# Performance work log

Hardware: AMD Instinct MI355X
Metric: run time of the kernel (lower is better)

## Reference

```python
import jax, jax.numpy as jnp
import numpy as np

B, N, E = 16, 10000, 160000
C_IN, C_SP, C_OUT = 32, 16, 32


def _glorot(key, shape):
    s = float(np.sqrt(6.0 / (shape[0] + shape[1])))
    return jax.random.uniform(key, shape, jnp.float32, -s, s)


def setup_inputs() -> dict:
    key = jax.random.key(0)
    ks = jax.random.split(key, 12)
    X = jax.random.normal(ks[0], (B, N, C_IN), jnp.float32)
    edge_index1 = jax.random.randint(ks[1], (2, E), 0, N)
    edge_weight1 = jax.random.uniform(ks[2], (E,), jnp.float32)
    res_n_id1 = jnp.arange(N)
    edge_index2 = jax.random.randint(ks[3], (2, E), 0, N)
    edge_weight2 = jax.random.uniform(ks[4], (E,), jnp.float32)
    res_n_id2 = jnp.arange(N)
    # conv1 params (in=C_IN, out=C_SP, edge_channels=1, concat=True)
    amp_w1 = _glorot(ks[5], (1, C_IN))            # [edge_ch, in]
    gate_w1 = _glorot(ks[6], (2 * C_IN + 1, 1))   # Linear(2*in+edge_ch, 1)
    gate_b1 = jnp.zeros((1,), jnp.float32)
    w1 = _glorot(ks[7], (2 * C_IN, C_SP))         # concat weight
    b1 = jnp.zeros((C_SP,), jnp.float32)
    # conv2 params (in=C_SP, out=C_OUT)
    amp_w2 = _glorot(ks[8], (1, C_SP))
    gate_w2 = _glorot(ks[9], (2 * C_SP + 1, 1))
    gate_b2 = jnp.zeros((1,), jnp.float32)
    w2 = _glorot(ks[10], (2 * C_SP, C_OUT))
    b2 = jnp.zeros((C_OUT,), jnp.float32)
    return dict(X=X, edge_index1=edge_index1, edge_weight1=edge_weight1, res_n_id1=res_n_id1,
                edge_index2=edge_index2, edge_weight2=edge_weight2, res_n_id2=res_n_id2,
                amp_w1=amp_w1, gate_w1=gate_w1, gate_b1=gate_b1, w1=w1, b1=b1,
                amp_w2=amp_w2, gate_w2=gate_w2, gate_b2=gate_b2, w2=w2, b2=b2)


def _sagela(x_src, x_dst, edge_index, edge_weight, amp_w, gate_w, gate_b, w, b):
    # x_src: [B, N_src, C], x_dst: [B, N_dst, C]
    src, dst = edge_index[0], edge_index[1]
    n_dst = x_dst.shape[1]
    C = x_src.shape[-1]
    x_j = x_src[:, src]                       # [B, E, C] gathered source feats
    x_i = x_dst[:, dst]                       # [B, E, C] gathered target feats
    e = edge_weight[:, None]                  # [E, 1] edge features
    # gate_linear(cat[x_i, x_j, e]) split into three matmuls (same math)
    wg_i, wg_j, wg_e = gate_w[:C], gate_w[C:2 * C], gate_w[2 * C:]
    lamb = jax.nn.sigmoid(x_i @ wg_i + x_j @ wg_j + (e @ wg_e)[None] + gate_b)  # [B, E, 1]
    amp = e @ amp_w                           # [E, C] edge amplification
    msg = amp[None, :, :] * x_j * lamb        # [B, E, C]
    # mean aggregation over incoming edges (scatter-add / count)
    aggr = jnp.zeros((x_src.shape[0], n_dst, C), msg.dtype).at[:, dst].add(msg)
    cnt = jnp.zeros((n_dst,), msg.dtype).at[dst].add(1.0)
    aggr = aggr / jnp.maximum(cnt, 1.0)[None, :, None]
    out = jnp.concatenate([x_dst, aggr], axis=-1) @ w + b  # [B, N_dst, out]
    return out


def reference(X, edge_index1, edge_weight1, res_n_id1, edge_index2, edge_weight2, res_n_id2,
              amp_w1, gate_w1, gate_b1, w1, b1, amp_w2, gate_w2, gate_b2, w2, b2):
    h = _sagela(X, X[:, res_n_id1], edge_index1, edge_weight1, amp_w1, gate_w1, gate_b1, w1, b1)
    h = jax.nn.leaky_relu(h, 0.01)
    out = _sagela(h, h[:, res_n_id2], edge_index2, edge_weight2, amp_w2, gate_w2, gate_b2, w2, b2)
    return out
```

## Files before the change

### kernel.cpp

```cpp
#include <hip/hip_runtime.h>
#include <math.h>

#define B 16
#define N 10000
#define E 160000
#define CAP 96

__device__ __forceinline__ ushort f2bf(float v) {
    uint u = __float_as_uint(v);
    u = (u + 0x7fffu + ((u >> 16) & 1u)) >> 16;
    return (ushort)u;
}
__device__ __forceinline__ float bf2f(ushort u) { return __uint_as_float(((uint)u) << 16); }
__device__ __forceinline__ float bf2f_lo(uint u) { return __uint_as_float(u << 16); }
__device__ __forceinline__ float bf2f_hi(uint u) { return __uint_as_float(u & 0xffff0000u); }
__device__ __forceinline__ float dec_ew(uint u) {
    return ((float)(u >> 14) + 0.5f) * (1.0f / 262144.0f);
}

__global__ __launch_bounds__(256)
void prep_bucket_kernel(const float* __restrict__ X,
                        const float* __restrict__ gate_w1,
                        const int* __restrict__ ei1, const float* __restrict__ ew1,
                        const int* __restrict__ ei2, const float* __restrict__ ew2,
                        const float* __restrict__ w1,
                        const float* __restrict__ w2,
                        ushort* __restrict__ xt,
                        float* __restrict__ gi, float* __restrict__ gj,
                        float* __restrict__ w1T, float* __restrict__ w2T,
                        int* __restrict__ bcount1, uint* __restrict__ bucket1,
                        int* __restrict__ bcount2, uint* __restrict__ bucket2) {
    int gtid = blockIdx.x * 256 + threadIdx.x;
    int gs = gridDim.x * 256;

    for (int t = gtid; t < 2 * E; t += gs) {
        if (t < E) {
            int d = ei1[E + t];
            int pos = atomicAdd(&bcount1[d], 1);
            if (pos < CAP) {
                uint q = (uint)(ew1[t] * 262144.0f);
                if (q > 262143u) q = 262143u;
                bucket1[d * CAP + pos] = (q << 14) | (uint)ei1[t];
            }
        } else {
            int e = t - E;
            int d = ei2[E + e];
            int pos = atomicAdd(&bcount2[d], 1);
            if (pos < CAP) {
                uint q = (uint)(ew2[e] * 262144.0f);
                if (q > 262143u) q = 262143u;
                bucket2[d * CAP + pos] = (q << 14) | (uint)ei2[e];
            }
        }
    }

    for (int tile = blockIdx.x; tile < N / 16; tile += gridDim.x) {
        int n0 = tile * 16;
        int nl = threadIdx.x >> 4, b = threadIdx.x & 15;
        int n = n0 + nl;
        const float4* xr = (const float4*)(X + ((size_t)b * N + n) * 32);
        float pi = 0.f, pj = 0.f;
        union { uint u[16]; uint4 v4[4]; } pk;
        #pragma unroll
        for (int q = 0; q < 8; ++q) {
            float4 v = xr[q];
            pi += v.x * gate_w1[4*q]   + v.y * gate_w1[4*q+1]
                + v.z * gate_w1[4*q+2] + v.w * gate_w1[4*q+3];
            pj += v.x * gate_w1[32+4*q]   + v.y * gate_w1[32+4*q+1]
                + v.z * gate_w1[32+4*q+2] + v.w * gate_w1[32+4*q+3];
            pk.u[2*q]   = (uint)f2bf(v.x) | ((uint)f2bf(v.y) << 16);
            pk.u[2*q+1] = (uint)f2bf(v.z) | ((uint)f2bf(v.w) << 16);
        }
        int r = n0 * 16 + threadIdx.x;
        uint4* dst = (uint4*)(xt + (size_t)r * 32);
        dst[0] = pk.v4[0]; dst[1] = pk.v4[1];
        dst[2] = pk.v4[2]; dst[3] = pk.v4[3];
        gi[r] = pi; gj[r] = pj;
    }

    if (gtid < 1024) {
        w1T[(gtid & 15) * 64 + (gtid >> 4)] = w1[gtid];
        w2T[(gtid & 31) * 32 + (gtid >> 5)] = w2[gtid];
    }
}

__global__ __launch_bounds__(256, 8)
void agg_dense1_kernel(const float* __restrict__ X,
                       const uint4* __restrict__ xt4,
                       const float* __restrict__ gi,
                       const float* __restrict__ gj,
                       const int* __restrict__ bcount,
                       const uint* __restrict__ bucket,
                       const float* __restrict__ gate_w,
                       const float* __restrict__ gate_b,
                       const float* __restrict__ amp_w,
                       const float* __restrict__ w1T,
                       const float* __restrict__ b1,
                       const float* __restrict__ gate_w2,
                       ushort* __restrict__ htb,
                       float* __restrict__ gi2, float* __restrict__ gj2) {
    __shared__ uint  s_eb[CAP];
    __shared__ float s_coef[CAP * 16];
    __shared__ float s_gi[16];
    __shared__ __align__(16) float s_x[16][36];
    __shared__ __align__(16) float s_feat[16][36];
    __shared__ __align__(16) float s_wmT[16 * 68];

    int n = blockIdx.x;
    int tid = threadIdx.x;

    int cnt = bcount[n];
    int deg = cnt < CAP ? cnt : CAP;
    if (tid < CAP / 4)
        ((uint4*)s_eb)[tid] = ((const uint4*)(bucket + (size_t)n * CAP))[tid];
    {
        int o = tid >> 4, k4 = tid & 15;
        *(float4*)&s_wmT[o * 68 + k4 * 4] = ((const float4*)w1T)[o * 16 + k4];
    }
    if (tid < 128) {
        int b = tid >> 3, q = tid & 7;
        *(float4*)&s_x[b][q * 4] = ((const float4*)(X + ((size_t)b * N + n) * 32))[q];
    }
    if (tid < 16) s_gi[tid] = gi[n * 16 + tid] + gate_b[0];
    __syncthreads();

    float wge = gate_w[64];
    for (int p = tid; p < deg * 16; p += 256) {
        int k = p >> 4, b = p & 15;
        uint pr = s_eb[k];
        float w = dec_ew(pr);
        float z = s_gi[b] + gj[(pr & 0x3FFFu) * 16 + b] + w * wge;
        s_coef[p] = w / (1.0f + __expf(-z));
    }
    __syncthreads();

    int wv = tid >> 6, l = tid & 63;
    int c8 = l & 3;
    int b  = 4 * wv + ((l >> 2) & 3);
    int h  = l >> 4;
    uint boff = (uint)b * 4 + c8;
    float a0 = 0.f, a1 = 0.f, a2 = 0.f, a3 = 0.f;
    float a4 = 0.f, a5 = 0.f, a6 = 0.f, a7 = 0.f;
    int k = h;
    for (; k + 4 < deg; k += 16) {
        bool v2 = (k + 8) < deg, v3 = (k + 12) < deg;
        uint i2 = v2 ? (uint)(k + 8) : 0u;
        uint i3 = v3 ? (uint)(k + 12) : 0u;
        uint p0 = s_eb[k], p1 = s_eb[k + 4], p2 = s_eb[i2], p3 = s_eb[i3];
        float c0 = s_coef[(k << 4) | b];
        float c1 = s_coef[((k + 4) << 4) | b];
        float c2 = s_coef[(i2 << 4) | b]; if (!v2) c2 = 0.f;
        float c3 = s_coef[(i3 << 4) | b]; if (!v3) c3 = 0.f;
        uint4 u0 = xt4[(p0 & 0x3FFFu) * 64u + boff];
        uint4 u1 = xt4[(p1 & 0x3FFFu) * 64u + boff];
        uint4 u2 = xt4[(p2 & 0x3FFFu) * 64u + boff];
        uint4 u3 = xt4[(p3 & 0x3FFFu) * 64u + boff];
        a0 += c0 * bf2f_lo(u0.x) + c1 * bf2f_lo(u1.x) + c2 * bf2f_lo(u2.x) + c3 * bf2f_lo(u3.x);
        a1 += c0 * bf2f_hi(u0.x) + c1 * bf2f_hi(u1.x) + c2 * bf2f_hi(u2.x) + c3 * bf2f_hi(u3.x);
        a2 += c0 * bf2f_lo(u0.y) + c1 * bf2f_lo(u1.y) + c2 * bf2f_lo(u2.y) + c3 * bf2f_lo(u3.y);
        a3 += c0 * bf2f_hi(u0.y) + c1 * bf2f_hi(u1.y) + c2 * bf2f_hi(u2.y) + c3 * bf2f_hi(u3.y);
        a4 += c0 * bf2f_lo(u0.z) + c1 * bf2f_lo(u1.z) + c2 * bf2f_lo(u2.z) + c3 * bf2f_lo(u3.z);
        a5 += c0 * bf2f_hi(u0.z) + c1 * bf2f_hi(u1.z) + c2 * bf2f_hi(u2.z) + c3 * bf2f_hi(u3.z);
        a6 += c0 * bf2f_lo(u0.w) + c1 * bf2f_lo(u1.w) + c2 * bf2f_lo(u2.w) + c3 * bf2f_lo(u3.w);
        a7 += c0 * bf2f_hi(u0.w) + c1 * bf2f_hi(u1.w) + c2 * bf2f_hi(u2.w) + c3 * bf2f_hi(u3.w);
    }
    if (k < deg) {
        uint pr = s_eb[k];
        float cc = s_coef[(k << 4) | b];
        uint4 u = xt4[(pr & 0x3FFFu) * 64u + boff];
        a0 += cc * bf2f_lo(u.x); a1 += cc * bf2f_hi(u.x);
        a2 += cc * bf2f_lo(u.y); a3 += cc * bf2f_hi(u.y);
        a4 += cc * bf2f_lo(u.z); a5 += cc * bf2f_hi(u.z);
        a6 += cc * bf2f_lo(u.w); a7 += cc * bf2f_hi(u.w);
    }
    a0 += __shfl_xor(a0, 16, 64); a0 += __shfl_xor(a0, 32, 64);
    a1 += __shfl_xor(a1, 16, 64); a1 += __shfl_xor(a1, 32, 64);
    a2 += __shfl_xor(a2, 16, 64); a2 += __shfl_xor(a2, 32, 64);
    a3 += __shfl_xor(a3, 16, 64); a3 += __shfl_xor(a3, 32, 64);
    a4 += __shfl_xor(a4, 16, 64); a4 += __shfl_xor(a4, 32, 64);
    a5 += __shfl_xor(a5, 16, 64); a5 += __shfl_xor(a5, 32, 64);
    a6 += __shfl_xor(a6, 16, 64); a6 += __shfl_xor(a6, 32, 64);
    a7 += __shfl_xor(a7, 16, 64); a7 += __shfl_xor(a7, 32, 64);
    if (h == 0) {
        float inv = 1.0f / fmaxf((float)cnt, 1.0f);
        int cb = 8 * c8;
        s_feat[b][cb]     = a0 * amp_w[cb]     * inv;
        s_feat[b][cb + 1] = a1 * amp_w[cb + 1] * inv;
        s_feat[b][cb + 2] = a2 * amp_w[cb + 2] * inv;
        s_feat[b][cb + 3] = a3 * amp_w[cb + 3] * inv;
        s_feat[b][cb + 4] = a4 * amp_w[cb + 4] * inv;
        s_feat[b][cb + 5] = a5 * amp_w[cb + 5] * inv;
        s_feat[b][cb + 6] = a6 * amp_w[cb + 6] * inv;
        s_feat[b][cb + 7] = a7 * amp_w[cb + 7] * inv;
    }
    __syncthreads();

    {
        int o = tid & 15, bb = tid >> 4;
        const float4* wr4 = (const float4*)&s_wmT[o * 68];
        const float4* x4  = (const float4*)&s_x[bb][0];
        const float4* f4  = (const float4*)&s_feat[bb][0];
        float d = b1[o];
        #pragma unroll
        for (int q = 0; q < 8; ++q) {
            float4 wvv = wr4[q],    xv = x4[q];
            float4 wf = wr4[8 + q], fv = f4[q];
            d += xv.x * wvv.x + xv.y * wvv.y + xv.z * wvv.z + xv.w * wvv.w;
            d += fv.x * wf.x + fv.y * wf.y + fv.z * wf.z + fv.w * wf.w;
        }
        d = d > 0.0f ? d : 0.01f * d;
        htb[((size_t)n * 16 + bb) * 16 + o] = f2bf(d);
        float pi = d * gate_w2[o];
        float pj = d * gate_w2[16 + o];
        #pragma unroll
        for (int off = 8; off; off >>= 1) {
            pi += __shfl_xor(pi, off, 16);
            pj += __shfl_xor(pj, off, 16);
        }
        if (o == 0) { gi2[n * 16 + bb] = pi; gj2[n * 16 + bb] = pj; }
    }
}

__global__ __launch_bounds__(256, 8)
void agg_dense2_kernel(const uint4* __restrict__ htb4,
                       const float* __restrict__ gi,
                       const float* __restrict__ gj,
                       const int* __restrict__ bcount,
                       const uint* __restrict__ bucket,
                       const float* __restrict__ gate_w,
                       const float* __restrict__ gate_b,
                       const float* __restrict__ amp_w,
                       const float* __restrict__ w2T,
                       const float* __restrict__ b2,
                       float* __restrict__ out) {
    __shared__ uint  s_eb[CAP];
    __shared__ float s_coef[CAP * 16];
    __shared__ float s_gi[16];
    __shared__ __align__(16) float s_x[16][20];
    __shared__ __align__(16) float s_feat[16][20];
    __shared__ __align__(16) float s_wmT[32 * 36];

    int n = blockIdx.x;
    int tid = threadIdx.x;

    int cnt = bcount[n];
    int deg = cnt < CAP ? cnt : CAP;
    if (tid < CAP / 4)
        ((uint4*)s_eb)[tid] = ((const uint4*)(bucket + (size_t)n * CAP))[tid];
    {
        int o = tid >> 3, k4 = tid & 7;
        *(float4*)&s_wmT[o * 36 + k4 * 4] = ((const float4*)w2T)[o * 8 + k4];
    }
    if (tid < 32) {
        uint4 u = htb4[(size_t)n * 32 + tid];
        int b = tid >> 1, cb = (tid & 1) * 8;
        float4 f0, f1;
        f0.x = bf2f_lo(u.x); f0.y = bf2f_hi(u.x);
        f0.z = bf2f_lo(u.y); f0.w = bf2f_hi(u.y);
        f1.x = bf2f_lo(u.z); f1.y = bf2f_hi(u.z);
        f1.z = bf2f_lo(u.w); f1.w = bf2f_hi(u.w);
        *(float4*)&s_x[b][cb]     = f0;
        *(float4*)&s_x[b][cb + 4] = f1;
    }
    if (tid < 16) s_gi[tid] = gi[n * 16 + tid] + gate_b[0];
    __syncthreads();

    float wge = gate_w[32];
    for (int p = tid; p < deg * 16; p += 256) {
        int k = p >> 4, b = p & 15;
        uint pr = s_eb[k];
        float w = dec_ew(pr);
        float z = s_gi[b] + gj[(pr & 0x3FFFu) * 16 + b] + w * wge;
        s_coef[p] = w / (1.0f + __expf(-z));
    }
    __syncthreads();

    int wv = tid >> 6, l = tid & 63;
    int c8 = l & 1;
    int b  = 4 * wv + ((l >> 1) & 3);
    int qd = l >> 3;
    uint boff = (uint)b * 2 + c8;
    float a0 = 0.f, a1 = 0.f, a2 = 0.f, a3 = 0.f;
    float a4 = 0.f, a5 = 0.f, a6 = 0.f, a7 = 0.f;
    int k = qd;
    for (; k + 8 < deg; k += 32) {
        bool v2 = (k + 16) < deg, v3 = (k + 24) < deg;
        uint i2 = v2 ? (uint)(k + 16) : 0u;
        uint i3 = v3 ? (uint)(k + 24) : 0u;
        uint p0 = s_eb[k], p1 = s_eb[k + 8], p2 = s_eb[i2], p3 = s_eb[i3];
        float c0 = s_coef[(k << 4) | b];
        float c1 = s_coef[((k + 8) << 4) | b];
        float c2 = s_coef[(i2 << 4) | b]; if (!v2) c2 = 0.f;
        float c3 = s_coef[(i3 << 4) | b]; if (!v3) c3 = 0.f;
        uint4 u0 = htb4[(p0 & 0x3FFFu) * 32u + boff];
        uint4 u1 = htb4[(p1 & 0x3FFFu) * 32u + boff];
        uint4 u2 = htb4[(p2 & 0x3FFFu) * 32u + boff];
        uint4 u3 = htb4[(p3 & 0x3FFFu) * 32u + boff];
        a0 += c0 * bf2f_lo(u0.x) + c1 * bf2f_lo(u1.x) + c2 * bf2f_lo(u2.x) + c3 * bf2f_lo(u3.x);
        a1 += c0 * bf2f_hi(u0.x) + c1 * bf2f_hi(u1.x) + c2 * bf2f_hi(u2.x) + c3 * bf2f_hi(u3.x);
        a2 += c0 * bf2f_lo(u0.y) + c1 * bf2f_lo(u1.y) + c2 * bf2f_lo(u2.y) + c3 * bf2f_lo(u3.y);
        a3 += c0 * bf2f_hi(u0.y) + c1 * bf2f_hi(u1.y) + c2 * bf2f_hi(u2.y) + c3 * bf2f_hi(u3.y);
        a4 += c0 * bf2f_lo(u0.z) + c1 * bf2f_lo(u1.z) + c2 * bf2f_lo(u2.z) + c3 * bf2f_lo(u3.z);
        a5 += c0 * bf2f_hi(u0.z) + c1 * bf2f_hi(u1.z) + c2 * bf2f_hi(u2.z) + c3 * bf2f_hi(u3.z);
        a6 += c0 * bf2f_lo(u0.w) + c1 * bf2f_lo(u1.w) + c2 * bf2f_lo(u2.w) + c3 * bf2f_lo(u3.w);
        a7 += c0 * bf2f_hi(u0.w) + c1 * bf2f_hi(u1.w) + c2 * bf2f_hi(u2.w) + c3 * bf2f_hi(u3.w);
    }
    if (k < deg) {
        uint pr = s_eb[k];
        float cc = s_coef[(k << 4) | b];
        uint4 u = htb4[(pr & 0x3FFFu) * 32u + boff];
        a0 += cc * bf2f_lo(u.x); a1 += cc * bf2f_hi(u.x);
        a2 += cc * bf2f_lo(u.y); a3 += cc * bf2f_hi(u.y);
        a4 += cc * bf2f_lo(u.z); a5 += cc * bf2f_hi(u.z);
        a6 += cc * bf2f_lo(u.w); a7 += cc * bf2f_hi(u.w);
    }
    a0 += __shfl_xor(a0, 8, 64); a0 += __shfl_xor(a0, 16, 64); a0 += __shfl_xor(a0, 32, 64);
    a1 += __shfl_xor(a1, 8, 64); a1 += __shfl_xor(a1, 16, 64); a1 += __shfl_xor(a1, 32, 64);
    a2 += __shfl_xor(a2, 8, 64); a2 += __shfl_xor(a2, 16, 64); a2 += __shfl_xor(a2, 32, 64);
    a3 += __shfl_xor(a3, 8, 64); a3 += __shfl_xor(a3, 16, 64); a3 += __shfl_xor(a3, 32, 64);
    a4 += __shfl_xor(a4, 8, 64); a4 += __shfl_xor(a4, 16, 64); a4 += __shfl_xor(a4, 32, 64);
    a5 += __shfl_xor(a5, 8, 64); a5 += __shfl_xor(a5, 16, 64); a5 += __shfl_xor(a5, 32, 64);
    a6 += __shfl_xor(a6, 8, 64); a6 += __shfl_xor(a6, 16, 64); a6 += __shfl_xor(a6, 32, 64);
    a7 += __shfl_xor(a7, 8, 64); a7 += __shfl_xor(a7, 16, 64); a7 += __shfl_xor(a7, 32, 64);
    if (qd == 0) {
        float inv = 1.0f / fmaxf((float)cnt, 1.0f);
        int cb = 8 * c8;
        s_feat[b][cb]     = a0 * amp_w[cb]     * inv;
        s_feat[b][cb + 1] = a1 * amp_w[cb + 1] * inv;
        s_feat[b][cb + 2] = a2 * amp_w[cb + 2] * inv;
        s_feat[b][cb + 3] = a3 * amp_w[cb + 3] * inv;
        s_feat[b][cb + 4] = a4 * amp_w[cb + 4] * inv;
        s_feat[b][cb + 5] = a5 * amp_w[cb + 5] * inv;
        s_feat[b][cb + 6] = a6 * amp_w[cb + 6] * inv;
        s_feat[b][cb + 7] = a7 * amp_w[cb + 7] * inv;
    }
    __syncthreads();

    {
        int o2 = tid & 15, bb = tid >> 4;
        const float4* wr0 = (const float4*)&s_wmT[(2 * o2) * 36];
        const float4* wr1 = (const float4*)&s_wmT[(2 * o2 + 1) * 36];
        const float4* x4  = (const float4*)&s_x[bb][0];
        const float4* f4  = (const float4*)&s_feat[bb][0];
        float d0 = b2[2 * o2], d1 = b2[2 * o2 + 1];
        #pragma unroll
        for (int q = 0; q < 4; ++q) {
            float4 xv = x4[q], fv = f4[q];
            float4 w0a = wr0[q], w0b = wr0[4 + q];
            float4 w1a = wr1[q], w1b = wr1[4 + q];
            d0 += xv.x * w0a.x + xv.y * w0a.y + xv.z * w0a.z + xv.w * w0a.w;
            d0 += fv.x * w0b.x + fv.y * w0b.y + fv.z * w0b.z + fv.w * w0b.w;
            d1 += xv.x * w1a.x + xv.y * w1a.y + xv.z * w1a.z + xv.w * w1a.w;
            d1 += fv.x * w1b.x + fv.y * w1b.y + fv.z * w1b.z + fv.w * w1b.w;
        }
        size_t ob = ((size_t)bb * N + n) * 32;
        float2 r; r.x = d0; r.y = d1;
        *(float2*)(out + ob + 2 * o2) = r;
    }
}

extern "C" void kernel_launch(void* const* d_in, const int* in_sizes, int n_in,
                              void* d_out, int out_size, void* d_ws, size_t ws_size,
                              hipStream_t stream) {
    const float* X       = (const float*)d_in[0];
    const int*   ei1     = (const int*)  d_in[1];
    const float* ew1     = (const float*)d_in[2];
    const int*   ei2     = (const int*)  d_in[4];
    const float* ew2     = (const float*)d_in[5];
    const float* amp_w1  = (const float*)d_in[7];
    const float* gate_w1 = (const float*)d_in[8];
    const float* gate_b1 = (const float*)d_in[9];
    const float* w1      = (const float*)d_in[10];
    const float* b1      = (const float*)d_in[11];
    const float* amp_w2  = (const float*)d_in[12];
    const float* gate_w2 = (const float*)d_in[13];
    const float* gate_b2 = (const float*)d_in[14];
    const float* w2      = (const float*)d_in[15];
    const float* b2      = (const float*)d_in[16];
    float* out = (float*)d_out;

    char* p = (char*)d_ws;
    ushort* xt     = (ushort*)p; p += (size_t)N * B * 32 * sizeof(ushort);
    ushort* htb    = (ushort*)p; p += (size_t)N * B * 16 * sizeof(ushort);
    float* gi1     = (float*)p;  p += (size_t)N * B * sizeof(float);
    float* gj1     = (float*)p;  p += (size_t)N * B * sizeof(float);
    float* gi2     = (float*)p;  p += (size_t)N * B * sizeof(float);
    float* gj2     = (float*)p;  p += (size_t)N * B * sizeof(float);
    uint*  bucket1 = (uint*)p;   p += (size_t)N * CAP * sizeof(uint);
    uint*  bucket2 = (uint*)p;   p += (size_t)N * CAP * sizeof(uint);
    int*   bcount1 = (int*)p;    p += (size_t)N * sizeof(int);
    int*   bcount2 = (int*)p;    p += (size_t)N * sizeof(int);
    float* w1T     = (float*)p;  p += 1024 * sizeof(float);
    float* w2T     = (float*)p;  p += 1024 * sizeof(float);

    hipMemsetAsync(bcount1, 0, 2 * (size_t)N * sizeof(int), stream);
    prep_bucket_kernel<<<2048, 256, 0, stream>>>(
        X, gate_w1, ei1, ew1, ei2, ew2, w1, w2, xt, gi1, gj1, w1T, w2T,
        bcount1, bucket1, bcount2, bucket2);

    agg_dense1_kernel<<<N, 256, 0, stream>>>(
        X, (const uint4*)xt, gi1, gj1, bcount1, bucket1,
        gate_w1, gate_b1, amp_w1, w1T, b1, gate_w2, htb, gi2, gj2);

    agg_dense2_kernel<<<N, 256, 0, stream>>>(
        (const uint4*)htb, gi2, gj2, bcount2, bucket2,
        gate_w2, gate_b2, amp_w2, w2T, b2, out);
}
```

Measured before the change: 200.6 us.

## Project layer-1 features through weights before aggregation to halve gathered width

Layer 1's linear map is now applied before the gather, not after. Each node's X is pre-multiplied in the prep kernel by the amp-scaled aggregate half of w1, giving a 16-wide bf16 table, plus the self half with bias, giving a 16-wide fp32 table. The per-destination aggregation therefore gathers 16 channels per edge instead of 32, and the per-block dense matmul and its shared-memory staging are removed. The cost is more arithmetic and an extra fp32 table write in the prep kernel. Rounding also changes, because the projected values rather than the raw X are quantized to bf16.

```diff
diff --git a/kernel.cpp b/kernel.cpp
--- a/kernel.cpp
+++ b/kernel.cpp
@@ -21,16 +21,27 @@
 __global__ __launch_bounds__(256)
 void prep_bucket_kernel(const float* __restrict__ X,
                         const float* __restrict__ gate_w1,
+                        const float* __restrict__ amp_w1,
+                        const float* __restrict__ b1,
                         const int* __restrict__ ei1, const float* __restrict__ ew1,
                         const int* __restrict__ ei2, const float* __restrict__ ew2,
                         const float* __restrict__ w1,
                         const float* __restrict__ w2,
-                        ushort* __restrict__ xt,
+                        ushort* __restrict__ yt,
+                        float* __restrict__ xpart,
                         float* __restrict__ gi, float* __restrict__ gj,
-                        float* __restrict__ w1T, float* __restrict__ w2T,
+                        float* __restrict__ w2T,
                         int* __restrict__ bcount1, uint* __restrict__ bucket1,
                         int* __restrict__ bcount2, uint* __restrict__ bucket2) {
-    int gtid = blockIdx.x * 256 + threadIdx.x;
+    __shared__ __align__(16) float s_w1[64 * 16];
+    int tid = threadIdx.x;
+    {
+        int i = tid * 4;
+        *(float4*)&s_w1[i] = *(const float4*)&w1[i];
+    }
+    __syncthreads();
+
+    int gtid = blockIdx.x * 256 + tid;
     int gs = gridDim.x * 256;
 
     for (int t = gtid; t < 2 * E; t += gs) {
@@ -54,13 +65,21 @@
         }
     }
 
+    if (gtid < 1024) {
+        w2T[(gtid & 31) * 32 + (gtid >> 5)] = w2[gtid];
+    }
+
     for (int tile = blockIdx.x; tile < N / 16; tile += gridDim.x) {
         int n0 = tile * 16;
-        int nl = threadIdx.x >> 4, b = threadIdx.x & 15;
+        int nl = tid >> 4, b = tid & 15;
         int n = n0 + nl;
-        const float4* xr = (const float4*)(X + ((size_t)b * N + n) * 32);
+        const float4* xr4 = (const float4*)(X + ((size_t)b * N + n) * 32);
+        float4 xr[8];
+        #pragma unroll
+        for (int q = 0; q < 8; ++q) xr[q] = xr4[q];
+        const float* xs = (const float*)xr;
+
         float pi = 0.f, pj = 0.f;
-        union { uint u[16]; uint4 v4[4]; } pk;
         #pragma unroll
         for (int q = 0; q < 8; ++q) {
             float4 v = xr[q];
@@ -68,43 +87,58 @@
                 + v.z * gate_w1[4*q+2] + v.w * gate_w1[4*q+3];
             pj += v.x * gate_w1[32+4*q]   + v.y * gate_w1[32+4*q+1]
                 + v.z * gate_w1[32+4*q+2] + v.w * gate_w1[32+4*q+3];
-            pk.u[2*q]   = (uint)f2bf(v.x) | ((uint)f2bf(v.y) << 16);
-            pk.u[2*q+1] = (uint)f2bf(v.z) | ((uint)f2bf(v.w) << 16);
         }
-        int r = n0 * 16 + threadIdx.x;
-        uint4* dst = (uint4*)(xt + (size_t)r * 32);
-        dst[0] = pk.v4[0]; dst[1] = pk.v4[1];
-        dst[2] = pk.v4[2]; dst[3] = pk.v4[3];
+
+        float po[16], py[16];
+        #pragma unroll
+        for (int o = 0; o < 16; ++o) { po[o] = b1[o]; py[o] = 0.f; }
+        #pragma unroll
+        for (int c = 0; c < 32; ++c) {
+            float xa = xs[c];
+            float ya = amp_w1[c] * xa;
+            const float4* wa = (const float4*)&s_w1[c * 16];
+            const float4* wb = (const float4*)&s_w1[(32 + c) * 16];
+            #pragma unroll
+            for (int q = 0; q < 4; ++q) {
+                float4 a = wa[q], bb = wb[q];
+                po[4*q]   += xa * a.x;  py[4*q]   += ya * bb.x;
+                po[4*q+1] += xa * a.y;  py[4*q+1] += ya * bb.y;
+                po[4*q+2] += xa * a.z;  py[4*q+2] += ya * bb.z;
+                po[4*q+3] += xa * a.w;  py[4*q+3] += ya * bb.w;
+            }
+        }
+
+        int r = n0 * 16 + tid;
+        uint pk[8];
+        #pragma unroll
+        for (int j = 0; j < 8; ++j)
+            pk[j] = (uint)f2bf(py[2*j]) | ((uint)f2bf(py[2*j+1]) << 16);
+        uint4* yd = (uint4*)(yt + (size_t)r * 16);
+        yd[0] = make_uint4(pk[0], pk[1], pk[2], pk[3]);
+        yd[1] = make_uint4(pk[4], pk[5], pk[6], pk[7]);
+        float4* xd = (float4*)(xpart + (size_t)r * 16);
+        #pragma unroll
+        for (int q = 0; q < 4; ++q)
+            xd[q] = make_float4(po[4*q], po[4*q+1], po[4*q+2], po[4*q+3]);
         gi[r] = pi; gj[r] = pj;
     }
-
-    if (gtid < 1024) {
-        w1T[(gtid & 15) * 64 + (gtid >> 4)] = w1[gtid];
-        w2T[(gtid & 31) * 32 + (gtid >> 5)] = w2[gtid];
-    }
 }
 
 __global__ __launch_bounds__(256, 8)
-void agg_dense1_kernel(const float* __restrict__ X,
-                       const uint4* __restrict__ xt4,
-                       const float* __restrict__ gi,
-                       const float* __restrict__ gj,
-                       const int* __restrict__ bcount,
-                       const uint* __restrict__ bucket,
-                       const float* __restrict__ gate_w,
-                       const float* __restrict__ gate_b,
-                       const float* __restrict__ amp_w,
-                       const float* __restrict__ w1T,
-                       const float* __restrict__ b1,
-                       const float* __restrict__ gate_w2,
-                       ushort* __restrict__ htb,
-                       float* __restrict__ gi2, float* __restrict__ gj2) {
+void agg1_kernel(const uint4* __restrict__ y4,
+                 const float* __restrict__ xpart,
+                 const float* __restrict__ gi,
+                 const float* __restrict__ gj,
+                 const int* __restrict__ bcount,
+                 const uint* __restrict__ bucket,
+                 const float* __restrict__ gate_w,
+                 const float* __restrict__ gate_b,
+                 const float* __restrict__ gate_w2,
+                 ushort* __restrict__ htb,
+                 float* __restrict__ gi2, float* __restrict__ gj2) {
     __shared__ uint  s_eb[CAP];
     __shared__ float s_coef[CAP * 16];
     __shared__ float s_gi[16];
-    __shared__ __align__(16) float s_x[16][36];
-    __shared__ __align__(16) float s_feat[16][36];
-    __shared__ __align__(16) float s_wmT[16 * 68];
 
     int n = blockIdx.x;
     int tid = threadIdx.x;
@@ -113,14 +147,6 @@
     int deg = cnt < CAP ? cnt : CAP;
     if (tid < CAP / 4)
         ((uint4*)s_eb)[tid] = ((const uint4*)(bucket + (size_t)n * CAP))[tid];
-    {
-        int o = tid >> 4, k4 = tid & 15;
-        *(float4*)&s_wmT[o * 68 + k4 * 4] = ((const float4*)w1T)[o * 16 + k4];
-    }
-    if (tid < 128) {
-        int b = tid >> 3, q = tid & 7;
-        *(float4*)&s_x[b][q * 4] = ((const float4*)(X + ((size_t)b * N + n) * 32))[q];
-    }
     if (tid < 16) s_gi[tid] = gi[n * 16 + tid] + gate_b[0];
     __syncthreads();
 
@@ -135,89 +161,61 @@
     __syncthreads();
 
     int wv = tid >> 6, l = tid & 63;
-    int c8 = l & 3;
-    int b  = 4 * wv + ((l >> 2) & 3);
-    int h  = l >> 4;
-    uint boff = (uint)b * 4 + c8;
+    int og = l & 1;
+    int b  = 4 * wv + ((l >> 1) & 3);
+    int h  = l >> 3;
+    uint boff = (uint)b * 2 + og;
     float a0 = 0.f, a1 = 0.f, a2 = 0.f, a3 = 0.f;
     float a4 = 0.f, a5 = 0.f, a6 = 0.f, a7 = 0.f;
-    int k = h;
-    for (; k + 4 < deg; k += 16) {
-        bool v2 = (k + 8) < deg, v3 = (k + 12) < deg;
-        uint i2 = v2 ? (uint)(k + 8) : 0u;
-        uint i3 = v3 ? (uint)(k + 12) : 0u;
-        uint p0 = s_eb[k], p1 = s_eb[k + 4], p2 = s_eb[i2], p3 = s_eb[i3];
-        float c0 = s_coef[(k << 4) | b];
-        float c1 = s_coef[((k + 4) << 4) | b];
-        float c2 = s_coef[(i2 << 4) | b]; if (!v2) c2 = 0.f;
-        float c3 = s_coef[(i3 << 4) | b]; if (!v3) c3 = 0.f;
-        uint4 u0 = xt4[(p0 & 0x3FFFu) * 64u + boff];
-        uint4 u1 = xt4[(p1 & 0x3FFFu) * 64u + boff];
-        uint4 u2 = xt4[(p2 & 0x3FFFu) * 64u + boff];
-        uint4 u3 = xt4[(p3 & 0x3FFFu) * 64u + boff];
-        a0 += c0 * bf2f_lo(u0.x) + c1 * bf2f_lo(u1.x) + c2 * bf2f_lo(u2.x) + c3 * bf2f_lo(u3.x);
-        a1 += c0 * bf2f_hi(u0.x) + c1 * bf2f_hi(u1.x) + c2 * bf2f_hi(u2.x) + c3 * bf2f_hi(u3.x);
-        a2 += c0 * bf2f_lo(u0.y) + c1 * bf2f_lo(u1.y) + c2 * bf2f_lo(u2.y) + c3 * bf2f_lo(u3.y);
-        a3 += c0 * bf2f_hi(u0.y) + c1 * bf2f_hi(u1.y) + c2 * bf2f_hi(u2.y) + c3 * bf2f_hi(u3.y);
-        a4 += c0 * bf2f_lo(u0.z) + c1 * bf2f_lo(u1.z) + c2 * bf2f_lo(u2.z) + c3 * bf2f_lo(u3.z);
-        a5 += c0 * bf2f_hi(u0.z) + c1 * bf2f_hi(u1.z) + c2 * bf2f_hi(u2.z) + c3 * bf2f_hi(u3.z);
-        a6 += c0 * bf2f_lo(u0.w) + c1 * bf2f_lo(u1.w) + c2 * bf2f_lo(u2.w) + c3 * bf2f_lo(u3.w);
-        a7 += c0 * bf2f_hi(u0.w) + c1 * bf2f_hi(u1.w) + c2 * bf2f_hi(u2.w) + c3 * bf2f_hi(u3.w);
-    }
-    if (k < deg) {
+    for (int k = h; k < deg; k += 8) {
         uint pr = s_eb[k];
         float cc = s_coef[(k << 4) | b];
-        uint4 u = xt4[(pr & 0x3FFFu) * 64u + boff];
+        uint4 u = y4[(pr & 0x3FFFu) * 32u + boff];
         a0 += cc * bf2f_lo(u.x); a1 += cc * bf2f_hi(u.x);
         a2 += cc * bf2f_lo(u.y); a3 += cc * bf2f_hi(u.y);
         a4 += cc * bf2f_lo(u.z); a5 += cc * bf2f_hi(u.z);
         a6 += cc * bf2f_lo(u.w); a7 += cc * bf2f_hi(u.w);
     }
-    a0 += __shfl_xor(a0, 16, 64); a0 += __shfl_xor(a0, 32, 64);
-    a1 += __shfl_xor(a1, 16, 64); a1 += __shfl_xor(a1, 32, 64);
-    a2 += __shfl_xor(a2, 16, 64); a2 += __shfl_xor(a2, 32, 64);
-    a3 += __shfl_xor(a3, 16, 64); a3 += __shfl_xor(a3, 32, 64);
-    a4 += __shfl_xor(a4, 16, 64); a4 += __shfl_xor(a4, 32, 64);
-    a5 += __shfl_xor(a5, 16, 64); a5 += __shfl_xor(a5, 32, 64);
-    a6 += __shfl_xor(a6, 16, 64); a6 += __shfl_xor(a6, 32, 64);
-    a7 += __shfl_xor(a7, 16, 64); a7 += __shfl_xor(a7, 32, 64);
+    a0 += __shfl_xor(a0, 8, 64); a0 += __shfl_xor(a0, 16, 64); a0 += __shfl_xor(a0, 32, 64);
+    a1 += __shfl_xor(a1, 8, 64); a1 += __shfl_xor(a1, 16, 64); a1 += __shfl_xor(a1, 32, 64);
+    a2 += __shfl_xor(a2, 8, 64); a2 += __shfl_xor(a2, 16, 64); a2 += __shfl_xor(a2, 32, 64);
+    a3 += __shfl_xor(a3, 8, 64); a3 += __shfl_xor(a3, 16, 64); a3 += __shfl_xor(a3, 32, 64);
+    a4 += __shfl_xor(a4, 8, 64); a4 += __shfl_xor(a4, 16, 64); a4 += __shfl_xor(a4, 32, 64);
+    a5 += __shfl_xor(a5, 8, 64); a5 += __shfl_xor(a5, 16, 64); a5 += __shfl_xor(a5, 32, 64);
+    a6 += __shfl_xor(a6, 8, 64); a6 += __shfl_xor(a6, 16, 64); a6 += __shfl_xor(a6, 32, 64);
+    a7 += __shfl_xor(a7, 8, 64); a7 += __shfl_xor(a7, 16, 64); a7 += __shfl_xor(a7, 32, 64);
+
     if (h == 0) {
         float inv = 1.0f / fmaxf((float)cnt, 1.0f);
-        int cb = 8 * c8;
-        s_feat[b][cb]     = a0 * amp_w[cb]     * inv;
-        s_feat[b][cb + 1] = a1 * amp_w[cb + 1] * inv;
-        s_feat[b][cb + 2] = a2 * amp_w[cb + 2] * inv;
-        s_feat[b][cb + 3] = a3 * amp_w[cb + 3] * inv;
-        s_feat[b][cb + 4] = a4 * amp_w[cb + 4] * inv;
-        s_feat[b][cb + 5] = a5 * amp_w[cb + 5] * inv;
-        s_feat[b][cb + 6] = a6 * amp_w[cb + 6] * inv;
-        s_feat[b][cb + 7] = a7 * amp_w[cb + 7] * inv;
-    }
-    __syncthreads();
-
-    {
-        int o = tid & 15, bb = tid >> 4;
-        const float4* wr4 = (const float4*)&s_wmT[o * 68];
-        const float4* x4  = (const float4*)&s_x[bb][0];
-        const float4* f4  = (const float4*)&s_feat[bb][0];
-        float d = b1[o];
-        #pragma unroll
-        for (int q = 0; q < 8; ++q) {
-            float4 wvv = wr4[q],    xv = x4[q];
-            float4 wf = wr4[8 + q], fv = f4[q];
-            d += xv.x * wvv.x + xv.y * wvv.y + xv.z * wvv.z + xv.w * wvv.w;
-            d += fv.x * wf.x + fv.y * wf.y + fv.z * wf.z + fv.w * wf.w;
-        }
-        d = d > 0.0f ? d : 0.01f * d;
-        htb[((size_t)n * 16 + bb) * 16 + o] = f2bf(d);
-        float pi = d * gate_w2[o];
-        float pj = d * gate_w2[16 + o];
-        #pragma unroll
-        for (int off = 8; off; off >>= 1) {
-            pi += __shfl_xor(pi, off, 16);
-            pj += __shfl_xor(pj, off, 16);
-        }
-        if (o == 0) { gi2[n * 16 + bb] = pi; gj2[n * 16 + bb] = pj; }
+        size_t xb = ((size_t)n * 16 + b) * 16 + 8 * og;
+        float4 xp0 = *(const float4*)&xpart[xb];
+        float4 xp1 = *(const float4*)&xpart[xb + 4];
+        float v0 = xp0.x + inv * a0, v1 = xp0.y + inv * a1;
+        float v2 = xp0.z + inv * a2, v3 = xp0.w + inv * a3;
+        float v4 = xp1.x + inv * a4, v5 = xp1.y + inv * a5;
+        float v6 = xp1.z + inv * a6, v7 = xp1.w + inv * a7;
+        v0 = v0 > 0.f ? v0 : 0.01f * v0;  v1 = v1 > 0.f ? v1 : 0.01f * v1;
+        v2 = v2 > 0.f ? v2 : 0.01f * v2;  v3 = v3 > 0.f ? v3 : 0.01f * v3;
+        v4 = v4 > 0.f ? v4 : 0.01f * v4;  v5 = v5 > 0.f ? v5 : 0.01f * v5;
+        v6 = v6 > 0.f ? v6 : 0.01f * v6;  v7 = v7 > 0.f ? v7 : 0.01f * v7;
+        uint4 pk;
+        pk.x = (uint)f2bf(v0) | ((uint)f2bf(v1) << 16);
+        pk.y = (uint)f2bf(v2) | ((uint)f2bf(v3) << 16);
+        pk.z = (uint)f2bf(v4) | ((uint)f2bf(v5) << 16);
+        pk.w = (uint)f2bf(v6) | ((uint)f2bf(v7) << 16);
+        ((uint4*)htb)[(size_t)n * 32 + boff] = pk;
+        int ob = 8 * og;
+        float pi = v0 * gate_w2[ob]     + v1 * gate_w2[ob + 1]
+                 + v2 * gate_w2[ob + 2] + v3 * gate_w2[ob + 3]
+                 + v4 * gate_w2[ob + 4] + v5 * gate_w2[ob + 5]
+                 + v6 * gate_w2[ob + 6] + v7 * gate_w2[ob + 7];
+        float pj = v0 * gate_w2[16 + ob]     + v1 * gate_w2[16 + ob + 1]
+                 + v2 * gate_w2[16 + ob + 2] + v3 * gate_w2[16 + ob + 3]
+                 + v4 * gate_w2[16 + ob + 4] + v5 * gate_w2[16 + ob + 5]
+                 + v6 * gate_w2[16 + ob + 6] + v7 * gate_w2[16 + ob + 7];
+        pi += __shfl_xor(pi, 1, 64);
+        pj += __shfl_xor(pj, 1, 64);
+        if (og == 0) { gi2[n * 16 + b] = pi; gj2[n * 16 + b] = pj; }
     }
 }
 
@@ -380,8 +378,9 @@
     float* out = (float*)d_out;
 
     char* p = (char*)d_ws;
-    ushort* xt     = (ushort*)p; p += (size_t)N * B * 32 * sizeof(ushort);
+    ushort* yt     = (ushort*)p; p += (size_t)N * B * 16 * sizeof(ushort);
     ushort* htb    = (ushort*)p; p += (size_t)N * B * 16 * sizeof(ushort);
+    float* xpart   = (float*)p;  p += (size_t)N * B * 16 * sizeof(float);
     float* gi1     = (float*)p;  p += (size_t)N * B * sizeof(float);
     float* gj1     = (float*)p;  p += (size_t)N * B * sizeof(float);
     float* gi2     = (float*)p;  p += (size_t)N * B * sizeof(float);
@@ -390,17 +389,17 @@
     uint*  bucket2 = (uint*)p;   p += (size_t)N * CAP * sizeof(uint);
     int*   bcount1 = (int*)p;    p += (size_t)N * sizeof(int);
     int*   bcount2 = (int*)p;    p += (size_t)N * sizeof(int);
-    float* w1T     = (float*)p;  p += 1024 * sizeof(float);
     float* w2T     = (float*)p;  p += 1024 * sizeof(float);
 
     hipMemsetAsync(bcount1, 0, 2 * (size_t)N * sizeof(int), stream);
     prep_bucket_kernel<<<2048, 256, 0, stream>>>(
-        X, gate_w1, ei1, ew1, ei2, ew2, w1, w2, xt, gi1, gj1, w1T, w2T,
+        X, gate_w1, amp_w1, b1, ei1, ew1, ei2, ew2, w1, w2,
+        yt, xpart, gi1, gj1, w2T,
         bcount1, bucket1, bcount2, bucket2);
 
-    agg_dense1_kernel<<<N, 256, 0, stream>>>(
-        X, (const uint4*)xt, gi1, gj1, bcount1, bucket1,
-        gate_w1, gate_b1, amp_w1, w1T, b1, gate_w2, htb, gi2, gj2);
+    agg1_kernel<<<N, 256, 0, stream>>>(
+        (const uint4*)yt, xpart, gi1, gj1, bcount1, bucket1,
+        gate_w1, gate_b1, gate_w2, htb, gi2, gj2);
 
     agg_dense2_kernel<<<N, 256, 0, stream>>>(
         (const uint4*)htb, gi2, gj2, bcount2, bucket2,
```

Measured after the change: 206.4 us. 2.9% more time.
